# Performance work log

Measured on AMD Instinct MI355X. Metric: run time of the kernel, lower is better.

The kernel has to match this reference:

```python
import jax, jax.numpy as jnp
import numpy as np

B, S, Q, D = 8, 2048, 2048, 1024  # additive path requires S == Q


def setup_inputs() -> dict:
    key = jax.random.key(0)
    ks = jax.random.split(key, 5)
    def glorot(k, shape):
        fan_in, fan_out = shape[0], shape[1]
        limit = np.sqrt(6.0 / (fan_in + fan_out)).astype(np.float32)
        return jax.random.uniform(k, shape, jnp.float32, -limit, limit)
    return {
        "source": jax.random.normal(ks[0], (B, S, D), jnp.float32),
        "query": jax.random.normal(ks[1], (B, Q, D), jnp.float32),
        "kernel": glorot(ks[2], (S, Q)),
        "wk_kernel": glorot(ks[3], (D, Q)),
        "wq_kernel": glorot(ks[4], (S, D)),
    }


def reference(source, query, kernel, wk_kernel, wq_kernel):
    # query permuted to (B, D, Q) as in call()
    q_t = jnp.transpose(query, (0, 2, 1))
    # additive similarity: tanh(Wk . Source + Wq . Query) . kernel
    f_att = (jnp.einsum("bsd,dq->bsq", source, wk_kernel)
             + jnp.einsum("sd,bdq->bsq", wq_kernel, q_t))  # (B, S, Q)
    sim = jnp.einsum("bsq,qt->bst", jnp.tanh(f_att), kernel)  # (B, S, Q)
    sm = jax.nn.softmax(sim, axis=-1)  # softmax over last axis (Keras default)
    # sm_t = permute(sm, (0,2,1)); result = batch_dot(sm_t, Source)
    return jnp.einsum("bsq,bsd->bqd", sm, source)  # (B, Q, D)
```

## Files before the change

### kernel.cpp

```cpp
#include <hip/hip_runtime.h>
#include <hip/hip_bf16.h>
#include <stdint.h>

typedef unsigned short u16;

#define B_ 8
#define S_ 2048
#define Q_ 2048
#define D_ 1024
#define T_ 2048

typedef __attribute__((ext_vector_type(8))) short short8;
typedef __attribute__((ext_vector_type(4))) float f32x4;

__device__ __forceinline__ u16 f2b(float f) {
  union { float f; uint32_t u; } x; x.f = f;
  uint32_t r = x.u + 0x7fffu + ((x.u >> 16) & 1u);
  return (u16)(r >> 16);
}
__device__ __forceinline__ float b2f(u16 h) {
  union { uint32_t u; float f; } x; x.u = ((uint32_t)h) << 16;
  return x.f;
}
__device__ __forceinline__ float tanh_fast(float x) {
  return 1.0f - 2.0f / (__expf(2.0f * x) + 1.0f);
}
__device__ __forceinline__ void async16(const void* g, void* l) {
  __builtin_amdgcn_global_load_lds(
      (const __attribute__((address_space(1))) void*)g,
      (__attribute__((address_space(3))) void*)l, 16, 0, 0);
}

__global__ void cast_f32_bf16_k(const float* __restrict__ in, u16* __restrict__ out, int n4) {
  int i = blockIdx.x * 256 + threadIdx.x;
  if (i >= n4) return;
  float4 v = ((const float4*)in)[i];
  uint32_t lo = (uint32_t)f2b(v.x) | ((uint32_t)f2b(v.y) << 16);
  uint32_t hi = (uint32_t)f2b(v.z) | ((uint32_t)f2b(v.w) << 16);
  ((uint2*)out)[i] = make_uint2(lo, hi);
}

__global__ void transpose_f32_bf16_v(const float* __restrict__ in, u16* __restrict__ out,
                                     int R, int C) {
  __shared__ u16 t[64 * 72];
  int z = blockIdx.z;
  const float* pin = in + (size_t)z * R * C;
  u16* pout = out + (size_t)z * R * C;
  int c0 = blockIdx.x * 64, r0 = blockIdx.y * 64;
  int tid = threadIdx.x;
  int rr = tid >> 4, c4 = (tid & 15) * 4;
#pragma unroll
  for (int p = 0; p < 4; ++p) {
    int r = p * 16 + rr;
    float4 v = *(const float4*)&pin[(size_t)(r0 + r) * C + c0 + c4];
    t[(c4 + 0) * 72 + r] = f2b(v.x);
    t[(c4 + 1) * 72 + r] = f2b(v.y);
    t[(c4 + 2) * 72 + r] = f2b(v.z);
    t[(c4 + 3) * 72 + r] = f2b(v.w);
  }
  __syncthreads();
  int ct = tid >> 3, r8 = (tid & 7) * 8;
#pragma unroll
  for (int p = 0; p < 2; ++p) {
    int c = p * 32 + ct;
    uint2 lo = *(const uint2*)&t[c * 72 + r8];
    uint2 hi = *(const uint2*)&t[c * 72 + r8 + 4];
    *(uint4*)&pout[(size_t)(c0 + c) * R + r0 + r8] = make_uint4(lo.x, lo.y, hi.x, hi.y);
  }
}

__global__ void src_prep_v(const float* __restrict__ in, u16* __restrict__ outc,
                           u16* __restrict__ outT) {
  __shared__ u16 t[64 * 72];
  int z = blockIdx.z;
  const float* pin = in + (size_t)z * S_ * D_;
  u16* pc = outc + (size_t)z * S_ * D_;
  u16* pt = outT + (size_t)z * S_ * D_;
  int c0 = blockIdx.x * 64, r0 = blockIdx.y * 64;
  int tid = threadIdx.x;
  int rr = tid >> 4, c4 = (tid & 15) * 4;
#pragma unroll
  for (int p = 0; p < 4; ++p) {
    int r = p * 16 + rr;
    float4 v = *(const float4*)&pin[(size_t)(r0 + r) * D_ + c0 + c4];
    u16 b0 = f2b(v.x), b1 = f2b(v.y), b2 = f2b(v.z), b3 = f2b(v.w);
    uint2 pk;
    pk.x = (uint32_t)b0 | ((uint32_t)b1 << 16);
    pk.y = (uint32_t)b2 | ((uint32_t)b3 << 16);
    *(uint2*)&pc[(size_t)(r0 + r) * D_ + c0 + c4] = pk;
    t[(c4 + 0) * 72 + r] = b0;
    t[(c4 + 1) * 72 + r] = b1;
    t[(c4 + 2) * 72 + r] = b2;
    t[(c4 + 3) * 72 + r] = b3;
  }
  __syncthreads();
  int ct = tid >> 3, r8 = (tid & 7) * 8;
#pragma unroll
  for (int p = 0; p < 2; ++p) {
    int c = p * 32 + ct;
    uint2 lo = *(const uint2*)&t[c * 72 + r8];
    uint2 hi = *(const uint2*)&t[c * 72 + r8 + 4];
    *(uint4*)&pt[(size_t)(c0 + c) * S_ + r0 + r8] = make_uint4(lo.x, lo.y, hi.x, hi.y);
  }
}

__global__ void scale_srcT_k(u16* __restrict__ srcT, const float* __restrict__ l) {
  size_t i = (size_t)blockIdx.x * 256 + threadIdx.x;
  size_t e0 = i * 8;
  int s8 = (int)(e0 & (S_ - 1));
  int bb = (int)(e0 / ((size_t)D_ * S_));
  const float* lp = l + (size_t)bb * S_ + s8;
  float4 l0 = *(const float4*)lp;
  float4 l1 = *(const float4*)(lp + 4);
  uint4 raw = *(uint4*)&srcT[e0];
  uint32_t w[4] = {raw.x, raw.y, raw.z, raw.w};
  float li[8] = {l0.x, l0.y, l0.z, l0.w, l1.x, l1.y, l1.z, l1.w};
  uint32_t o[4];
#pragma unroll
  for (int k = 0; k < 4; ++k) {
    float a = b2f((u16)(w[k] & 0xffffu)) / li[2 * k];
    float b = b2f((u16)(w[k] >> 16)) / li[2 * k + 1];
    o[k] = (uint32_t)f2b(a) | ((uint32_t)f2b(b) << 16);
  }
  *(uint4*)&srcT[e0] = make_uint4(o[0], o[1], o[2], o[3]);
}

__global__ __launch_bounds__(512, 2) void gemm256_k(
    const u16* __restrict__ A1, long lda1, long bsA1,
    const u16* __restrict__ B1, long ldb1, long bsB1,
    const u16* __restrict__ A2, long lda2, long bsA2,
    const u16* __restrict__ B2, long ldb2, long bsB2,
    void* __restrict__ Cv, long ldc, long bsC,
    int K, int Srows, int nTerms, int mode, float* __restrict__ lsum) {
  __shared__ __align__(16) u16 lds[65536];

  const int tid = threadIdx.x;
  const int w = tid >> 6, lane = tid & 63;
  const int wr = w >> 2, wc = w & 3;
  const int l15 = lane & 15, lhi4 = lane >> 4;

  const int gx = gridDim.x;
  const int nwg = gx * (int)gridDim.y;
  int lid = blockIdx.y * gx + blockIdx.x;
  if ((nwg & 7) == 0) lid = (lid & 7) * (nwg >> 3) + (lid >> 3);
  const int bn = lid % gx, bm = lid / gx;
  const int n0 = bn * 256, m0 = bm * 256;
  const int b = m0 / Srows;
  const int s0 = m0 - b * Srows;

  const int ktiles = K >> 6;
  const int ktlog = __ffs(ktiles) - 1;
  const int ktmask = ktiles - 1;
  const int NT = nTerms * ktiles;

  const u16* gA1 = A1 + (size_t)bsA1 * b + (size_t)s0 * lda1;
  const u16* gB1 = B1 + (size_t)bsB1 * b + (size_t)n0 * ldb1;
  const u16* gA2 = (nTerms > 1) ? (A2 + (size_t)bsA2 * b + (size_t)s0 * lda2) : gA1;
  const u16* gB2 = (nTerms > 1) ? (B2 + (size_t)bsB2 * b + (size_t)n0 * ldb2) : gB1;

  const int lrow = lane >> 3;
  const int gk = ((lane & 7) ^ ((lane >> 5) << 1)) * 8;

  auto STG = [&](int tile, int isB, int half) {
    if (tile >= NT) return;
    const int term = tile >> ktlog;
    const int kt = (tile & ktmask) << 6;
    const u16* g = isB ? (term ? gB2 : gB1) : (term ? gA2 : gA1);
    const long ld = isB ? (term ? ldb2 : ldb1) : (term ? lda2 : lda1);
    u16* lb = lds + (tile & 1) * 32768 + isB * 16384;
#pragma unroll
    for (int is = 0; is < 2; ++is) {
      const int ci = is * 8 + w;
      const int r0 = isB ? ((ci >> 2) * 64 + half * 32 + (ci & 3) * 8)
                         : (is * 128 + half * 64 + w * 8);
      async16(g + (size_t)(r0 + lrow) * ld + kt + gk, lb + r0 * 64);
    }
  };

  f32x4 acc[8][4];
#pragma unroll
  for (int x = 0; x < 8; ++x)
#pragma unroll
    for (int y = 0; y < 4; ++y)
#pragma unroll
      for (int r = 0; r < 4; ++r) acc[x][y][r] = 0.0f;

  u16* bufXA = lds;
  u16* bufXB = lds + 16384;
  u16* bufYA = lds + 32768;
  u16* bufYB = lds + 49152;

  const int rsx = ((l15 >> 2) & 1) << 4;
  const int aBase = (((wr * 128 + l15) * 64) + lhi4 * 8) ^ rsx;
  const int bBase = (((wc * 64 + l15) * 64) + lhi4 * 8) ^ rsx;

  short8 av[4][2], bv[2][2];

#define RD_A(bufA, mh)                                                         \
  _Pragma("unroll") for (int kk = 0; kk < 2; ++kk)                             \
  _Pragma("unroll") for (int fr = 0; fr < 4; ++fr)                             \
      av[fr][kk] = *(const short8*)&(bufA)[aBase + (mh)*4096 + fr * 1024 + kk * 32];
#define RD_B(bufB, bp)                                                         \
  _Pragma("unroll") for (int kk = 0; kk < 2; ++kk)                             \
  _Pragma("unroll") for (int fc = 0; fc < 2; ++fc)                             \
      bv[fc][kk] = *(const short8*)&(bufB)[bBase + (bp)*2048 + fc * 1024 + kk * 32];
#define BAR __builtin_amdgcn_s_barrier()
#define SB0 __builtin_amdgcn_sched_barrier(0)
#define LGKM0 asm volatile("s_waitcnt lgkmcnt(0)")
#define VMC4 asm volatile("s_waitcnt vmcnt(4)" ::: "memory")
#define VMC0 asm volatile("s_waitcnt vmcnt(0)" ::: "memory")
#define MFMA16(mh, bp)                                                         \
  __builtin_amdgcn_s_setprio(1);                                               \
  _Pragma("unroll") for (int kk = 0; kk < 2; ++kk)                             \
  _Pragma("unroll") for (int fr = 0; fr < 4; ++fr)                             \
  _Pragma("unroll") for (int fc = 0; fc < 2; ++fc)                             \
      acc[(mh)*4 + fr][(bp)*2 + fc] = __builtin_amdgcn_mfma_f32_16x16x32_bf16( \
          av[fr][kk], bv[fc][kk], acc[(mh)*4 + fr][(bp)*2 + fc], 0, 0, 0);     \
  __builtin_amdgcn_s_setprio(0)

  STG(0, 0, 0); STG(0, 1, 1); STG(0, 0, 1); STG(0, 1, 0);
  STG(1, 0, 0); STG(1, 1, 1);
  VMC4;
  BAR; SB0;

  const int niter = NT >> 1;
  for (int i = 0; i + 1 < niter; ++i) {
    const int u = 2 * i;
    RD_A(bufXA, 0); RD_B(bufXB, 0);
    STG(u + 1, 0, 1);
    BAR; LGKM0; SB0;
    MFMA16(0, 0);
    BAR;

    RD_B(bufXB, 1);
    STG(u + 1, 1, 0);
    BAR; LGKM0; SB0;
    MFMA16(0, 1);
    BAR;

    RD_A(bufXA, 1);
    STG(u + 2, 0, 0);
    BAR; LGKM0; SB0;
    MFMA16(1, 1);
    BAR;

    RD_B(bufXB, 0);
    STG(u + 2, 1, 1);
    BAR; LGKM0; SB0;
    MFMA16(1, 0);
    VMC4;
    BAR; SB0;

    RD_A(bufYA, 0); RD_B(bufYB, 0);
    STG(u + 2, 0, 1);
    BAR; LGKM0; SB0;
    MFMA16(0, 0);
    BAR;

    RD_B(bufYB, 1);
    STG(u + 2, 1, 0);
    BAR; LGKM0; SB0;
    MFMA16(0, 1);
    BAR;

    RD_A(bufYA, 1);
    STG(u + 3, 0, 0);
    BAR; LGKM0; SB0;
    MFMA16(1, 1);
    BAR;

    RD_B(bufYB, 0);
    STG(u + 3, 1, 1);
    BAR; LGKM0; SB0;
    MFMA16(1, 0);
    VMC4;
    BAR; SB0;
  }

  {
    RD_A(bufXA, 0); RD_B(bufXB, 0);
    STG(NT - 1, 0, 1);
    BAR; LGKM0; SB0;
    MFMA16(0, 0);
    BAR;

    RD_B(bufXB, 1);
    STG(NT - 1, 1, 0);
    BAR; LGKM0; SB0;
    MFMA16(0, 1);
    BAR;

    RD_A(bufXA, 1);
    BAR; LGKM0; SB0;
    MFMA16(1, 1);
    BAR;

    RD_B(bufXB, 0);
    BAR; LGKM0; SB0;
    MFMA16(1, 0);
    VMC0;
    BAR; SB0;

    RD_A(bufYA, 0); RD_B(bufYB, 0);
    BAR; LGKM0; SB0;
    MFMA16(0, 0);
    BAR;

    RD_B(bufYB, 1);
    BAR; LGKM0; SB0;
    MFMA16(0, 1);
    BAR;

    RD_A(bufYA, 1);
    BAR; LGKM0; SB0;
    MFMA16(1, 1);
    BAR;

    RD_B(bufYB, 0);
    BAR; LGKM0; SB0;
    MFMA16(1, 0);
  }

  if (mode == 3) {
#pragma unroll
    for (int fr = 0; fr < 8; ++fr)
#pragma unroll
      for (int fc = 0; fc < 4; ++fc)
#pragma unroll
        for (int r = 0; r < 4; ++r) acc[fr][fc][r] = __expf(acc[fr][fc][r]);
    float* lrowp = lsum + (size_t)b * Srows + s0;
#pragma unroll
    for (int fr = 0; fr < 8; ++fr)
#pragma unroll
      for (int r = 0; r < 4; ++r) {
        float pv = acc[fr][0][r] + acc[fr][1][r] + acc[fr][2][r] + acc[fr][3][r];
        pv += __shfl_xor(pv, 1);
        pv += __shfl_xor(pv, 2);
        pv += __shfl_xor(pv, 4);
        pv += __shfl_xor(pv, 8);
        if (l15 == 0) {
          const int row = wr * 128 + fr * 16 + lhi4 * 4 + r;
          atomicAdd(&lrowp[row], pv);
        }
      }
    u16* gP = (u16*)Cv + (size_t)bsC * b + (size_t)n0 * ldc + s0;
    __syncthreads();
#pragma unroll
    for (int p = 0; p < 2; ++p) {
      if ((wc >> 1) == p) {
#pragma unroll
        for (int fr = 0; fr < 8; ++fr)
#pragma unroll
          for (int fc = 0; fc < 4; ++fc) {
            const int tc = (wc & 1) * 64 + fc * 16 + l15;
            const int sl = wr * 128 + fr * 16 + lhi4 * 4;
            u16 p0 = f2b(acc[fr][fc][0]);
            u16 p1 = f2b(acc[fr][fc][1]);
            u16 p2 = f2b(acc[fr][fc][2]);
            u16 p3 = f2b(acc[fr][fc][3]);
            uint2 pk;
            pk.x = (uint32_t)p0 | ((uint32_t)p1 << 16);
            pk.y = (uint32_t)p2 | ((uint32_t)p3 << 16);
            *(uint2*)&lds[tc * 268 + sl] = pk;
          }
      }
      __syncthreads();
#pragma unroll
      for (int j = 0; j < 8; ++j) {
        const int idx = j * 512 + tid;
        const int tt = idx >> 5, s8 = (idx & 31) * 8;
        uint2 lo = *(const uint2*)&lds[tt * 268 + s8];
        uint2 h2 = *(const uint2*)&lds[tt * 268 + s8 + 4];
        *(uint4*)&gP[(size_t)(p * 128 + tt) * ldc + s8] =
            make_uint4(lo.x, lo.y, h2.x, h2.y);
      }
      __syncthreads();
    }
    return;
  }

  const size_t cb = (size_t)bsC * b + (size_t)s0 * ldc + n0;
  if (mode == 2) {
    float* C = (float*)Cv + cb;
#pragma unroll
    for (int fr = 0; fr < 8; ++fr)
#pragma unroll
      for (int fc = 0; fc < 4; ++fc) {
        const int col = wc * 64 + fc * 16 + l15;
#pragma unroll
        for (int r = 0; r < 4; ++r) {
          const int row = wr * 128 + fr * 16 + lhi4 * 4 + r;
          C[(size_t)row * ldc + col] = acc[fr][fc][r];
        }
      }
  } else {
    u16* C = (u16*)Cv + cb;
#pragma unroll
    for (int fr = 0; fr < 8; ++fr)
#pragma unroll
      for (int fc = 0; fc < 4; ++fc) {
        const int col = wc * 64 + fc * 16 + l15;
#pragma unroll
        for (int r = 0; r < 4; ++r) {
          const int row = wr * 128 + fr * 16 + lhi4 * 4 + r;
          float v = acc[fr][fc][r];
          if (mode == 0) v = tanh_fast(v);
          C[(size_t)row * ldc + col] = f2b(v);
        }
      }
  }
}

#undef RD_A
#undef RD_B
#undef BAR
#undef SB0
#undef LGKM0
#undef VMC4
#undef VMC0
#undef MFMA16

extern "C" void kernel_launch(void* const* d_in, const int* in_sizes, int n_in,
                              void* d_out, int out_size, void* d_ws, size_t ws_size,
                              hipStream_t stream) {
  const float* src = (const float*)d_in[0];
  const float* qry = (const float*)d_in[1];
  const float* ker = (const float*)d_in[2];
  const float* wk  = (const float*)d_in[3];
  const float* wq  = (const float*)d_in[4];
  float* out = (float*)d_out;
  u16* ws = (u16*)d_ws;

  u16* srcb  = ws;
  u16* qryb  = srcb  + (size_t)B_ * S_ * D_;
  u16* wqb   = qryb  + (size_t)B_ * Q_ * D_;
  u16* wkT   = wqb   + (size_t)S_ * D_;
  u16* kerT  = wkT   + (size_t)D_ * Q_;
  u16* srcT  = kerT  + (size_t)Q_ * T_;
  u16* tanhT = srcT  + (size_t)B_ * D_ * S_;
  u16* PT    = tanhT + (size_t)B_ * S_ * Q_;
  float* l   = (float*)(PT + (size_t)B_ * T_ * S_);

  dim3 tb(256);

  cast_f32_bf16_k<<<(B_ * Q_ * D_) / 1024, 256, 0, stream>>>(qry, qryb, (B_ * Q_ * D_) / 4);
  cast_f32_bf16_k<<<(S_ * D_) / 1024, 256, 0, stream>>>(wq, wqb, (S_ * D_) / 4);
  transpose_f32_bf16_v<<<dim3(Q_ / 64, D_ / 64, 1), tb, 0, stream>>>(wk, wkT, D_, Q_);
  transpose_f32_bf16_v<<<dim3(T_ / 64, Q_ / 64, 1), tb, 0, stream>>>(ker, kerT, Q_, T_);
  src_prep_v<<<dim3(D_ / 64, S_ / 64, B_), tb, 0, stream>>>(src, srcb, srcT);
  hipMemsetAsync(l, 0, (size_t)B_ * S_ * sizeof(float), stream);

  gemm256_k<<<dim3(Q_ / 256, (B_ * S_) / 256), 512, 0, stream>>>(
      srcb, D_, (long)S_ * D_,
      wkT, D_, 0,
      wqb, D_, 0,
      qryb, D_, (long)Q_ * D_,
      tanhT, Q_, (long)S_ * Q_,
      D_, S_, 2, 0, nullptr);

  gemm256_k<<<dim3(T_ / 256, (B_ * S_) / 256), 512, 0, stream>>>(
      tanhT, Q_, (long)S_ * Q_,
      kerT, Q_, 0,
      nullptr, 0, 0, nullptr, 0, 0,
      PT, S_, (long)T_ * S_,
      Q_, S_, 1, 3, l);

  scale_srcT_k<<<(B_ * D_ * S_) / (256 * 8), 256, 0, stream>>>(srcT, l);

  gemm256_k<<<dim3(D_ / 256, (B_ * T_) / 256), 512, 0, stream>>>(
      PT, S_, (long)T_ * S_,
      srcT, S_, (long)D_ * S_,
      nullptr, 0, 0, nullptr, 0, 0,
      out, D_, (long)T_ * D_,
      S_, T_, 1, 2, nullptr);
}
```

Measured before the change: 602.9 us.

## Store LDS tiles in MFMA fragment order and load all B fragments once

Global-to-LDS async copies now write each 16-row by 32-k slab contiguously in fragment order, so every lane reads its short8 at lane*8. This removes the XOR swizzle and gives conflict-free linear LDS reads. B fragments for both column halves are now read once per buffer instead of twice, which cuts LDS read traffic. The cost is extra registers for the doubled bv array, which could hurt occupancy. The global load pattern also changes to 16-row by 64-byte segments, which may be less coalesced.

```diff
diff --git a/kernel.cpp b/kernel.cpp
--- a/kernel.cpp
+++ b/kernel.cpp
@@ -158,9 +158,6 @@
   const u16* gA2 = (nTerms > 1) ? (A2 + (size_t)bsA2 * b + (size_t)s0 * lda2) : gA1;
   const u16* gB2 = (nTerms > 1) ? (B2 + (size_t)bsB2 * b + (size_t)n0 * ldb2) : gB1;
 
-  const int lrow = lane >> 3;
-  const int gk = ((lane & 7) ^ ((lane >> 5) << 1)) * 8;
-
   auto STG = [&](int tile, int isB, int half) {
     if (tile >= NT) return;
     const int term = tile >> ktlog;
@@ -170,10 +167,12 @@
     u16* lb = lds + (tile & 1) * 32768 + isB * 16384;
 #pragma unroll
     for (int is = 0; is < 2; ++is) {
-      const int ci = is * 8 + w;
-      const int r0 = isB ? ((ci >> 2) * 64 + half * 32 + (ci & 3) * 8)
-                         : (is * 128 + half * 64 + w * 8);
-      async16(g + (size_t)(r0 + lrow) * ld + kt + gk, lb + r0 * 64);
+      const int bi = is * 8 + w;
+      int s, kk;
+      if (isB) { s = (bi >> 2) * 4 + half * 2 + (bi & 1); kk = (bi >> 1) & 1; }
+      else     { s = half * 4 + (bi & 3) + (bi >> 3) * 8; kk = (bi >> 2) & 1; }
+      async16(g + (size_t)(s * 16 + l15) * ld + kt + kk * 32 + lhi4 * 8,
+              lb + s * 1024 + kk * 512);
     }
   };
 
@@ -190,20 +189,21 @@
   u16* bufYA = lds + 32768;
   u16* bufYB = lds + 49152;
 
-  const int rsx = ((l15 >> 2) & 1) << 4;
-  const int aBase = (((wr * 128 + l15) * 64) + lhi4 * 8) ^ rsx;
-  const int bBase = (((wc * 64 + l15) * 64) + lhi4 * 8) ^ rsx;
-
-  short8 av[4][2], bv[2][2];
+  const int lof = lane * 8;
+
+  short8 av[4][2], bv[2][2][2];
 
 #define RD_A(bufA, mh)                                                         \
   _Pragma("unroll") for (int kk = 0; kk < 2; ++kk)                             \
   _Pragma("unroll") for (int fr = 0; fr < 4; ++fr)                             \
-      av[fr][kk] = *(const short8*)&(bufA)[aBase + (mh)*4096 + fr * 1024 + kk * 32];
-#define RD_B(bufB, bp)                                                         \
+      av[fr][kk] =                                                             \
+          *(const short8*)&(bufA)[(wr * 8 + (mh)*4 + fr) * 1024 + kk * 512 + lof];
+#define RD_B_ALL(bufB)                                                         \
+  _Pragma("unroll") for (int bp = 0; bp < 2; ++bp)                             \
+  _Pragma("unroll") for (int fc = 0; fc < 2; ++fc)                             \
   _Pragma("unroll") for (int kk = 0; kk < 2; ++kk)                             \
-  _Pragma("unroll") for (int fc = 0; fc < 2; ++fc)                             \
-      bv[fc][kk] = *(const short8*)&(bufB)[bBase + (bp)*2048 + fc * 1024 + kk * 32];
+      bv[bp][fc][kk] =                                                         \
+          *(const short8*)&(bufB)[(wc * 4 + bp * 2 + fc) * 1024 + kk * 512 + lof];
 #define BAR __builtin_amdgcn_s_barrier()
 #define SB0 __builtin_amdgcn_sched_barrier(0)
 #define LGKM0 asm volatile("s_waitcnt lgkmcnt(0)")
@@ -215,7 +215,7 @@
   _Pragma("unroll") for (int fr = 0; fr < 4; ++fr)                             \
   _Pragma("unroll") for (int fc = 0; fc < 2; ++fc)                             \
       acc[(mh)*4 + fr][(bp)*2 + fc] = __builtin_amdgcn_mfma_f32_16x16x32_bf16( \
-          av[fr][kk], bv[fc][kk], acc[(mh)*4 + fr][(bp)*2 + fc], 0, 0, 0);     \
+          av[fr][kk], bv[bp][fc][kk], acc[(mh)*4 + fr][(bp)*2 + fc], 0, 0, 0); \
   __builtin_amdgcn_s_setprio(0)
 
   STG(0, 0, 0); STG(0, 1, 1); STG(0, 0, 1); STG(0, 1, 0);
@@ -226,13 +226,12 @@
   const int niter = NT >> 1;
   for (int i = 0; i + 1 < niter; ++i) {
     const int u = 2 * i;
-    RD_A(bufXA, 0); RD_B(bufXB, 0);
+    RD_A(bufXA, 0); RD_B_ALL(bufXB);
     STG(u + 1, 0, 1);
     BAR; LGKM0; SB0;
     MFMA16(0, 0);
     BAR;
 
-    RD_B(bufXB, 1);
     STG(u + 1, 1, 0);
     BAR; LGKM0; SB0;
     MFMA16(0, 1);
@@ -244,20 +243,18 @@
     MFMA16(1, 1);
     BAR;
 
-    RD_B(bufXB, 0);
     STG(u + 2, 1, 1);
     BAR; LGKM0; SB0;
     MFMA16(1, 0);
     VMC4;
     BAR; SB0;
 
-    RD_A(bufYA, 0); RD_B(bufYB, 0);
+    RD_A(bufYA, 0); RD_B_ALL(bufYB);
     STG(u + 2, 0, 1);
     BAR; LGKM0; SB0;
     MFMA16(0, 0);
     BAR;
 
-    RD_B(bufYB, 1);
     STG(u + 2, 1, 0);
     BAR; LGKM0; SB0;
     MFMA16(0, 1);
@@ -269,7 +266,6 @@
     MFMA16(1, 1);
     BAR;
 
-    RD_B(bufYB, 0);
     STG(u + 3, 1, 1);
     BAR; LGKM0; SB0;
     MFMA16(1, 0);
@@ -278,13 +274,12 @@
   }
 
   {
-    RD_A(bufXA, 0); RD_B(bufXB, 0);
+    RD_A(bufXA, 0); RD_B_ALL(bufXB);
     STG(NT - 1, 0, 1);
     BAR; LGKM0; SB0;
     MFMA16(0, 0);
     BAR;
 
-    RD_B(bufXB, 1);
     STG(NT - 1, 1, 0);
     BAR; LGKM0; SB0;
     MFMA16(0, 1);
@@ -295,18 +290,16 @@
     MFMA16(1, 1);
     BAR;
 
-    RD_B(bufXB, 0);
     BAR; LGKM0; SB0;
     MFMA16(1, 0);
     VMC0;
     BAR; SB0;
 
-    RD_A(bufYA, 0); RD_B(bufYB, 0);
+    RD_A(bufYA, 0); RD_B_ALL(bufYB);
     BAR; LGKM0; SB0;
     MFMA16(0, 0);
     BAR;
 
-    RD_B(bufYB, 1);
     BAR; LGKM0; SB0;
     MFMA16(0, 1);
     BAR;
@@ -316,7 +309,6 @@
     MFMA16(1, 1);
     BAR;
 
-    RD_B(bufYB, 0);
     BAR; LGKM0; SB0;
     MFMA16(1, 0);
   }
@@ -412,7 +404,7 @@
 }
 
 #undef RD_A
-#undef RD_B
+#undef RD_B_ALL
 #undef BAR
 #undef SB0
 #undef LGKM0
```

Result: faster. 585.6 us (-2.9%).
